# Kernel optimization log

Hardware: AMD Instinct MI355X
Metric: run time of the kernel (lower is better)

The kernel has to match this reference:

```python
import jax, jax.numpy as jnp
import numpy as np

N_NODES = 100000
IN_FEATURES = 5000
OUT_FEATURES = 64
NNZ = 4000000


def setup_inputs() -> dict:
    key = jax.random.key(0)
    k_row, k_col, k_val, k_w, k_b = jax.random.split(key, 5)
    rows = jax.random.randint(k_row, (NNZ,), 0, N_NODES, dtype=jnp.int64 if jax.config.jax_enable_x64 else jnp.int32)
    cols = jax.random.randint(k_col, (NNZ,), 0, IN_FEATURES, dtype=rows.dtype)
    index = jnp.stack([rows, cols], axis=0)  # [2, nnz] COO
    value = jax.random.uniform(k_val, (NNZ,), dtype=jnp.float32)
    # kaiming_uniform_(mode='fan_out', a=sqrt(5)) on [in, out]: fan_out = out_features
    gain = np.sqrt(2.0 / (1.0 + 5.0))
    bound_w = gain * np.sqrt(3.0 / OUT_FEATURES)
    weight = jax.random.uniform(k_w, (IN_FEATURES, OUT_FEATURES), jnp.float32, -bound_w, bound_w)
    bound_b = 1.0 / np.sqrt(OUT_FEATURES)
    bias = jax.random.uniform(k_b, (OUT_FEATURES,), jnp.float32, -bound_b, bound_b)
    return {"index": index, "value": value, "n": N_NODES, "weight": weight, "bias": bias}


def reference(index, value, n, weight, bias):
    # spmm: out[r, :] = sum over nnz with row==r of value * weight[col, :]
    rows, cols = index[0], index[1]
    contrib = value[:, None] * weight[cols]            # [nnz, out] gather + scale
    res = jax.ops.segment_sum(contrib, rows, num_segments=n)  # [n, out] scatter-add
    return res + bias[None, :]
```

## Files before the change

kernel.cpp:

```cpp
#include <hip/hip_runtime.h>


#define NBF 1024
#define DMAX 128
#define CH 8192
#define CC 3072
#define SP_T 512
#define CSTR 16

__device__ __forceinline__ void ds_fadd(float* p, float v) {
    unsigned a = (unsigned)(unsigned long long)p;
    asm volatile("ds_add_f32 %0, %1" :: "v"(a), "v"(v) : "memory");
}

__global__ void k_init(int* __restrict__ cursorF, int* __restrict__ ovfCnt, int slots) {
    cursorF[threadIdx.x * CSTR] = threadIdx.x * slots;
    if (threadIdx.x == 0) *ovfCnt = 0;
}

__global__ __launch_bounds__(1024) void k_bin_fixed(const int* __restrict__ rows,
        const int* __restrict__ cols, const float* __restrict__ vals, int nnz,
        unsigned M, int S, int d, int slots, int* __restrict__ cursorF,
        unsigned long long* __restrict__ pairs1, int* __restrict__ ovfCnt,
        unsigned long long* __restrict__ ovf) {
    __shared__ unsigned long long stage[CH];
    __shared__ int histF[NBF], scF[NBF], adjF[NBF];
    __shared__ int wsum[16];
    int t = threadIdx.x, lane = t & 63, wv = t >> 6;
    long long base = (long long)blockIdx.x * CH;
    int count = (int)min((long long)CH, (long long)nnz - base);
    histF[t] = 0;
    __syncthreads();
    int f8[8], rk8[8];
    unsigned long long pk8[8];
#pragma unroll
    for (int k = 0; k < 8; ++k) {
        int i = t + (k << 10);
        f8[k] = -1;
        if (i < count) {
            unsigned r = (unsigned)rows[base + i];
            int c = cols[base + i];
            float vv = vals[base + i];
            int f = (int)(((unsigned long long)r * M) >> S);
            int lr = (int)r - f * d;
            f8[k] = f;
            rk8[k] = atomicAdd(&histF[f], 1);
            pk8[k] = ((unsigned long long)__float_as_uint(vv) << 32) |
                     ((unsigned)f << 20) | ((unsigned)lr << 13) | (unsigned)c;
        }
    }
    __syncthreads();
    int v = histF[t], x = v;
#pragma unroll
    for (int off = 1; off < 64; off <<= 1) {
        int y = __shfl_up(x, off, 64);
        if (lane >= off) x += y;
    }
    if (lane == 63) wsum[wv] = x;
    __syncthreads();
    if (t < 16) {
        int s = wsum[t], xs = s;
#pragma unroll
        for (int off = 1; off < 16; off <<= 1) {
            int y = __shfl_up(xs, off, 16);
            if (t >= off) xs += y;
        }
        wsum[t] = xs - s;
    }
    __syncthreads();
    int incl = x + wsum[wv];
    scF[t] = incl;
    if (v > 0) {
        int g = atomicAdd(&cursorF[t * CSTR], v);
        adjF[t] = g - (incl - v);
    }
    __syncthreads();
#pragma unroll
    for (int k = 0; k < 8; ++k)
        if (f8[k] >= 0) stage[(scF[f8[k]] - histF[f8[k]]) + rk8[k]] = pk8[k];
    __syncthreads();
    for (int i = t; i < count; i += 1024) {
        unsigned long long p = stage[i];
        int f = (int)((p >> 20) & 1023);
        int dest = adjF[f] + i;
        if (dest < (f + 1) * slots) pairs1[dest] = p;
        else ovf[atomicAdd(ovfCnt, 1)] = p;
    }
}

__global__ __launch_bounds__(SP_T, 6) void k_spmm9(
        const unsigned long long* __restrict__ pairs, const int* __restrict__ cursorF,
        const int* __restrict__ ovfCnt, const unsigned long long* __restrict__ ovf,
        const float* __restrict__ weight, const float* __restrict__ bias,
        float* __restrict__ out, int d, int n, int slots) {
    __shared__ unsigned long long stage[CC];
    __shared__ int histR[DMAX], scR[DMAX];
    extern __shared__ float acc[];
    int b = blockIdx.x, t = threadIdx.x;
    int row0 = b * d;
    if (row0 >= n) return;
    int nrows = min(d, n - row0);
    long long sbase = (long long)b * slots;
    int cnt = cursorF[b * CSTR] - (int)sbase;
    if (cnt > slots) cnt = slots;
    if (cnt < 0) cnt = 0;

    for (int i = t; i < (nrows << 6); i += SP_T) acc[i] = 0.0f;

    int g = t >> 4, fq = t & 15;
    for (int cb = 0; cb < cnt; cb += CC) {
        int ccnt = min(CC, cnt - cb);
        if (t < DMAX) histR[t] = 0;
        __syncthreads();
        int lr6[6], rk6[6];
        unsigned long long pk6[6];
#pragma unroll
        for (int k = 0; k < 6; ++k) {
            int i = t + (k << 9);
            lr6[k] = -1;
            if (i < ccnt) {
                unsigned long long p = pairs[sbase + cb + i];
                int lr = (int)((p >> 13) & 127);
                lr6[k] = lr;
                rk6[k] = atomicAdd(&histR[lr], 1);
                pk6[k] = p;
            }
        }
        __syncthreads();
        if (t < DMAX) {
            int v = histR[t], x = v;
            int lane = t & 63;
#pragma unroll
            for (int off = 1; off < 64; off <<= 1) {
                int y = __shfl_up(x, off, 64);
                if (lane >= off) x += y;
            }
            scR[t] = x;
        }
        __syncthreads();
        if (t >= 64 && t < DMAX) scR[t] += scR[63];
        __syncthreads();
#pragma unroll
        for (int k = 0; k < 6; ++k)
            if (lr6[k] >= 0) stage[(scR[lr6[k]] - histR[lr6[k]]) + rk6[k]] = pk6[k];
        __syncthreads();

        for (int r = g; r < nrows; r += 32) {
            int e = scR[r], s = e - histR[r];
            if (s >= e) continue;
            float4 a = {0.0f, 0.0f, 0.0f, 0.0f};
            int j = s;
            for (; j + 4 <= e; j += 4) {
                unsigned long long p0 = stage[j + 0];
                unsigned long long p1 = stage[j + 1];
                unsigned long long p2 = stage[j + 2];
                unsigned long long p3 = stage[j + 3];
                const float4 w0 = *(const float4*)(weight + (((int)(p0 & 8191)) << 6) + (fq << 2));
                const float4 w1 = *(const float4*)(weight + (((int)(p1 & 8191)) << 6) + (fq << 2));
                const float4 w2 = *(const float4*)(weight + (((int)(p2 & 8191)) << 6) + (fq << 2));
                const float4 w3 = *(const float4*)(weight + (((int)(p3 & 8191)) << 6) + (fq << 2));
                float v0 = __uint_as_float((unsigned)(p0 >> 32));
                float v1 = __uint_as_float((unsigned)(p1 >> 32));
                float v2 = __uint_as_float((unsigned)(p2 >> 32));
                float v3 = __uint_as_float((unsigned)(p3 >> 32));
                a.x = fmaf(v0, w0.x, a.x); a.y = fmaf(v0, w0.y, a.y);
                a.z = fmaf(v0, w0.z, a.z); a.w = fmaf(v0, w0.w, a.w);
                a.x = fmaf(v1, w1.x, a.x); a.y = fmaf(v1, w1.y, a.y);
                a.z = fmaf(v1, w1.z, a.z); a.w = fmaf(v1, w1.w, a.w);
                a.x = fmaf(v2, w2.x, a.x); a.y = fmaf(v2, w2.y, a.y);
                a.z = fmaf(v2, w2.z, a.z); a.w = fmaf(v2, w2.w, a.w);
                a.x = fmaf(v3, w3.x, a.x); a.y = fmaf(v3, w3.y, a.y);
                a.z = fmaf(v3, w3.z, a.z); a.w = fmaf(v3, w3.w, a.w);
            }
            for (; j < e; ++j) {
                unsigned long long p = stage[j];
                float vv = __uint_as_float((unsigned)(p >> 32));
                const float4 w = *(const float4*)(weight + (((int)(p & 8191)) << 6) + (fq << 2));
                a.x = fmaf(vv, w.x, a.x); a.y = fmaf(vv, w.y, a.y);
                a.z = fmaf(vv, w.z, a.z); a.w = fmaf(vv, w.w, a.w);
            }
            float4* ap = (float4*)&acc[(r << 6) + (fq << 2)];
            float4 o = *ap;
            o.x += a.x; o.y += a.y; o.z += a.z; o.w += a.w;
            *ap = o;
        }
        __syncthreads();
    }

    int oc = *ovfCnt;
    if (oc > 0) {
        __syncthreads();
        for (int i = g; i < oc; i += (SP_T >> 4)) {
            unsigned long long p = ovf[i];
            if ((int)((p >> 20) & 1023) == b) {
                int lr = (int)((p >> 13) & 127);
                int cc = (int)(p & 8191);
                float vv = __uint_as_float((unsigned)(p >> 32));
                const float4 w = *(const float4*)(weight + (cc << 6) + (fq << 2));
                float* ap = &acc[(lr << 6) + (fq << 2)];
                ds_fadd(ap + 0, vv * w.x); ds_fadd(ap + 1, vv * w.y);
                ds_fadd(ap + 2, vv * w.z); ds_fadd(ap + 3, vv * w.w);
            }
        }
        asm volatile("s_waitcnt lgkmcnt(0)" ::: "memory");
        __builtin_amdgcn_sched_barrier(0);
        __syncthreads();
    }

    for (int i = t; i < (nrows << 6); i += SP_T)
        out[((long long)row0 << 6) + i] = acc[i] + bias[i & 63];
}

extern "C" void kernel_launch(void* const* d_in, const int* in_sizes, int n_in,
                              void* d_out, int out_size, void* d_ws, size_t ws_size,
                              hipStream_t stream) {
    const int*   index  = (const int*)d_in[0];
    const float* value  = (const float*)d_in[1];
    const float* weight = (const float*)d_in[3];
    const float* bias   = (const float*)d_in[4];
    float*       out    = (float*)d_out;

    int nnz = in_sizes[0] / 2;
    int n   = out_size / 64;
    const int* rows = index;
    const int* cols = index + nnz;

    int d = (n + NBF - 1) / NBF;
    unsigned M = 0;
    int S = 0;
    for (S = 20; S <= 40; ++S) {
        unsigned long long m = ((1ull << S) + (unsigned)d - 1) / (unsigned)d;
        unsigned long long e = m * (unsigned long long)d - (1ull << S);
        if (m <= 0xffffffffull && e * (unsigned long long)(n > 0 ? n - 1 : 0) < (1ull << S)) {
            M = (unsigned)m;
            break;
        }
    }

    int nChunks = (nnz + CH - 1) / CH;
    char* ws = (char*)d_ws;
    int* cursorF = (int*)ws;
    int* ovfCnt  = (int*)(ws + (64 << 10));
    unsigned long long* pairsS = (unsigned long long*)(ws + (128 << 10));

    size_t szOvf = (((size_t)nnz * 8) + 255) & ~(size_t)255;
    size_t availS = (ws_size > (128 << 10) + szOvf) ? (ws_size - (128 << 10) - szOvf) : 0;
    long long slotsL = (long long)(availS / ((size_t)NBF * 8));
    int slots = (int)(slotsL > 6144 ? 6144 : slotsL);
    if (slots > 64) slots &= ~63;
    if (slots < 1) slots = 1;
    unsigned long long* ovf = (unsigned long long*)(ws + (128 << 10) + (size_t)slots * NBF * 8);

    k_init<<<1, 1024, 0, stream>>>(cursorF, ovfCnt, slots);
    k_bin_fixed<<<nChunks, 1024, 0, stream>>>(rows, cols, value, nnz, M, S, d, slots,
                                              cursorF, pairsS, ovfCnt, ovf);
    size_t smem = (size_t)d * 64 * sizeof(float);
    k_spmm9<<<NBF, SP_T, smem, stream>>>(pairsS, cursorF, ovfCnt, ovf, weight, bias,
                                         out, d, n, slots);
}
```

Measured before the change: 184.6 us.

## Split SpMM chunk work evenly across groups by nnz instead of by row

Each 16-thread group now processes an equal contiguous slice of the row-sorted staged nonzeros rather than whole rows. Partial sums for rows shared with neighbouring groups are added with LDS atomics, and interior rows use plain read-modify-write. This targets load imbalance from uneven row lengths. The chunk size is halved and the occupancy hint raised from 6 to 8 blocks per CU to reduce register and LDS pressure. The trade-off is more chunk iterations with extra barriers and some atomic LDS traffic.

```diff
diff --git a/kernel.cpp b/kernel.cpp
--- a/kernel.cpp
+++ b/kernel.cpp
@@ -4,7 +4,7 @@
 #define NBF 1024
 #define DMAX 128
 #define CH 8192
-#define CC 3072
+#define CC 1536
 #define SP_T 512
 #define CSTR 16
 
@@ -88,7 +88,7 @@
     }
 }
 
-__global__ __launch_bounds__(SP_T, 6) void k_spmm9(
+__global__ __launch_bounds__(SP_T, 8) void k_spmm11(
         const unsigned long long* __restrict__ pairs, const int* __restrict__ cursorF,
         const int* __restrict__ ovfCnt, const unsigned long long* __restrict__ ovf,
         const float* __restrict__ weight, const float* __restrict__ bias,
@@ -108,22 +108,24 @@
     for (int i = t; i < (nrows << 6); i += SP_T) acc[i] = 0.0f;
 
     int g = t >> 4, fq = t & 15;
+    const float* wbase = weight + (fq << 2);
+
     for (int cb = 0; cb < cnt; cb += CC) {
         int ccnt = min(CC, cnt - cb);
         if (t < DMAX) histR[t] = 0;
         __syncthreads();
-        int lr6[6], rk6[6];
-        unsigned long long pk6[6];
-#pragma unroll
-        for (int k = 0; k < 6; ++k) {
+        int lr3[3], rk3[3];
+        unsigned long long pk3[3];
+#pragma unroll
+        for (int k = 0; k < 3; ++k) {
             int i = t + (k << 9);
-            lr6[k] = -1;
+            lr3[k] = -1;
             if (i < ccnt) {
                 unsigned long long p = pairs[sbase + cb + i];
                 int lr = (int)((p >> 13) & 127);
-                lr6[k] = lr;
-                rk6[k] = atomicAdd(&histR[lr], 1);
-                pk6[k] = p;
+                lr3[k] = lr;
+                rk3[k] = atomicAdd(&histR[lr], 1);
+                pk3[k] = p;
             }
         }
         __syncthreads();
@@ -141,55 +143,72 @@
         if (t >= 64 && t < DMAX) scR[t] += scR[63];
         __syncthreads();
 #pragma unroll
-        for (int k = 0; k < 6; ++k)
-            if (lr6[k] >= 0) stage[(scR[lr6[k]] - histR[lr6[k]]) + rk6[k]] = pk6[k];
-        __syncthreads();
-
-        for (int r = g; r < nrows; r += 32) {
-            int e = scR[r], s = e - histR[r];
-            if (s >= e) continue;
+        for (int k = 0; k < 3; ++k)
+            if (lr3[k] >= 0) stage[(scR[lr3[k]] - histR[lr3[k]]) + rk3[k]] = pk3[k];
+        __syncthreads();
+
+        int Q = (ccnt + 31) >> 5;
+        int lo = g * Q, hi = min(lo + Q, ccnt);
+        if (lo < hi) {
+            int firstRow = (int)((stage[lo] >> 13) & 127);
+            int lastRow  = (int)((stage[hi - 1] >> 13) & 127);
+            int cr = firstRow;
             float4 a = {0.0f, 0.0f, 0.0f, 0.0f};
-            int j = s;
-            for (; j + 4 <= e; j += 4) {
-                unsigned long long p0 = stage[j + 0];
-                unsigned long long p1 = stage[j + 1];
-                unsigned long long p2 = stage[j + 2];
-                unsigned long long p3 = stage[j + 3];
-                const float4 w0 = *(const float4*)(weight + (((int)(p0 & 8191)) << 6) + (fq << 2));
-                const float4 w1 = *(const float4*)(weight + (((int)(p1 & 8191)) << 6) + (fq << 2));
-                const float4 w2 = *(const float4*)(weight + (((int)(p2 & 8191)) << 6) + (fq << 2));
-                const float4 w3 = *(const float4*)(weight + (((int)(p3 & 8191)) << 6) + (fq << 2));
-                float v0 = __uint_as_float((unsigned)(p0 >> 32));
-                float v1 = __uint_as_float((unsigned)(p1 >> 32));
-                float v2 = __uint_as_float((unsigned)(p2 >> 32));
-                float v3 = __uint_as_float((unsigned)(p3 >> 32));
-                a.x = fmaf(v0, w0.x, a.x); a.y = fmaf(v0, w0.y, a.y);
-                a.z = fmaf(v0, w0.z, a.z); a.w = fmaf(v0, w0.w, a.w);
-                a.x = fmaf(v1, w1.x, a.x); a.y = fmaf(v1, w1.y, a.y);
-                a.z = fmaf(v1, w1.z, a.z); a.w = fmaf(v1, w1.w, a.w);
-                a.x = fmaf(v2, w2.x, a.x); a.y = fmaf(v2, w2.y, a.y);
-                a.z = fmaf(v2, w2.z, a.z); a.w = fmaf(v2, w2.w, a.w);
-                a.x = fmaf(v3, w3.x, a.x); a.y = fmaf(v3, w3.y, a.y);
-                a.z = fmaf(v3, w3.z, a.z); a.w = fmaf(v3, w3.w, a.w);
-            }
-            for (; j < e; ++j) {
-                unsigned long long p = stage[j];
-                float vv = __uint_as_float((unsigned)(p >> 32));
-                const float4 w = *(const float4*)(weight + (((int)(p & 8191)) << 6) + (fq << 2));
-                a.x = fmaf(vv, w.x, a.x); a.y = fmaf(vv, w.y, a.y);
-                a.z = fmaf(vv, w.z, a.z); a.w = fmaf(vv, w.w, a.w);
-            }
-            float4* ap = (float4*)&acc[(r << 6) + (fq << 2)];
-            float4 o = *ap;
-            o.x += a.x; o.y += a.y; o.z += a.z; o.w += a.w;
-            *ap = o;
-        }
+            int j = lo;
+#define STEP(qv, wv4)                                                     \
+            {                                                             \
+                int lr_ = (int)(((qv) >> 13) & 127);                      \
+                if (lr_ != cr) {                                          \
+                    float* ap_ = &acc[(cr << 6) + (fq << 2)];             \
+                    if (cr == firstRow || cr == lastRow) {                \
+                        ds_fadd(ap_ + 0, a.x); ds_fadd(ap_ + 1, a.y);     \
+                        ds_fadd(ap_ + 2, a.z); ds_fadd(ap_ + 3, a.w);     \
+                    } else {                                              \
+                        float4 o_ = *(float4*)ap_;                        \
+                        o_.x += a.x; o_.y += a.y; o_.z += a.z; o_.w += a.w; \
+                        *(float4*)ap_ = o_;                               \
+                    }                                                     \
+                    a.x = 0.0f; a.y = 0.0f; a.z = 0.0f; a.w = 0.0f;       \
+                    cr = lr_;                                             \
+                }                                                         \
+                float vv_ = __uint_as_float((unsigned)((qv) >> 32));      \
+                a.x = fmaf(vv_, (wv4).x, a.x); a.y = fmaf(vv_, (wv4).y, a.y); \
+                a.z = fmaf(vv_, (wv4).z, a.z); a.w = fmaf(vv_, (wv4).w, a.w); \
+            }
+            for (; j + 4 <= hi; j += 4) {
+                unsigned long long q0 = stage[j + 0], q1 = stage[j + 1];
+                unsigned long long q2 = stage[j + 2], q3 = stage[j + 3];
+                const float4 w0 = *(const float4*)(wbase + ((int)(q0 & 8191) << 6));
+                const float4 w1 = *(const float4*)(wbase + ((int)(q1 & 8191) << 6));
+                const float4 w2 = *(const float4*)(wbase + ((int)(q2 & 8191) << 6));
+                const float4 w3 = *(const float4*)(wbase + ((int)(q3 & 8191) << 6));
+                STEP(q0, w0); STEP(q1, w1); STEP(q2, w2); STEP(q3, w3);
+            }
+            for (; j < hi; ++j) {
+                unsigned long long q = stage[j];
+                const float4 w = *(const float4*)(wbase + ((int)(q & 8191) << 6));
+                STEP(q, w);
+            }
+#undef STEP
+            {
+                float* ap_ = &acc[(cr << 6) + (fq << 2)];
+                if (cr == firstRow || cr == lastRow) {
+                    ds_fadd(ap_ + 0, a.x); ds_fadd(ap_ + 1, a.y);
+                    ds_fadd(ap_ + 2, a.z); ds_fadd(ap_ + 3, a.w);
+                } else {
+                    float4 o_ = *(float4*)ap_;
+                    o_.x += a.x; o_.y += a.y; o_.z += a.z; o_.w += a.w;
+                    *(float4*)ap_ = o_;
+                }
+            }
+        }
+        asm volatile("s_waitcnt lgkmcnt(0)" ::: "memory");
+        __builtin_amdgcn_sched_barrier(0);
         __syncthreads();
     }
 
     int oc = *ovfCnt;
     if (oc > 0) {
-        __syncthreads();
         for (int i = g; i < oc; i += (SP_T >> 4)) {
             unsigned long long p = ovf[i];
             if ((int)((p >> 20) & 1023) == b) {
@@ -204,8 +223,8 @@
         }
         asm volatile("s_waitcnt lgkmcnt(0)" ::: "memory");
         __builtin_amdgcn_sched_barrier(0);
-        __syncthreads();
-    }
+    }
+    __syncthreads();
 
     for (int i = t; i < (nrows << 6); i += SP_T)
         out[((long long)row0 << 6) + i] = acc[i] + bias[i & 63];
@@ -255,6 +274,6 @@
     k_bin_fixed<<<nChunks, 1024, 0, stream>>>(rows, cols, value, nnz, M, S, d, slots,
                                               cursorF, pairsS, ovfCnt, ovf);
     size_t smem = (size_t)d * 64 * sizeof(float);
-    k_spmm9<<<NBF, SP_T, smem, stream>>>(pairsS, cursorF, ovfCnt, ovf, weight, bias,
-                                         out, d, n, slots);
-}
+    k_spmm11<<<NBF, SP_T, smem, stream>>>(pairsS, cursorF, ovfCnt, ovf, weight, bias,
+                                          out, d, n, slots);
+}
```

New measurement: 211.4 us. 14.5% more time.
